# Kernel tuning notes

Measured on AMD Instinct MI355X. Metric: run time of the kernel, lower is better.

Reference implementation:

```python
import jax, jax.numpy as jnp
import numpy as np

B, S, D, H, F = 8, 1024, 1024, 16, 4096
DH = D // H  # 64
EPS = 1e-5


def layer_norm(x, g, b):
    mu = jnp.mean(x, axis=-1, keepdims=True)
    var = jnp.mean(jnp.square(x - mu), axis=-1, keepdims=True)
    return (x - mu) * jax.lax.rsqrt(var + EPS) * g + b


def mha(q_in, k_in, v_in, wq, wk, wv, wo, causal):
    # wq/wk/wv: [H, D, DH] (stacked per-head nn.Linear weights, pre-transposed)
    Q = jnp.einsum('bsd,hdk->bhsk', q_in, wq)
    K = jnp.einsum('bsd,hdk->bhsk', k_in, wk)
    V = jnp.einsum('bsd,hdk->bhsk', v_in, wv)
    scores = jnp.einsum('bhsk,bhtk->bhst', Q, K) / jnp.sqrt(jnp.asarray(DH, Q.dtype))
    if causal:
        mask = jnp.triu(jnp.ones((S, S), dtype=bool), k=1)  # True = inaccessible
        scores = jnp.where(mask, -jnp.inf, scores)
    A = jax.nn.softmax(scores, axis=-1)
    heads = jnp.einsum('bhst,bhtk->bhsk', A, V)
    heads = heads.transpose(0, 2, 1, 3).reshape(q_in.shape[0], q_in.shape[1], D)
    return heads @ wo.T  # nn.Linear convention


def setup_inputs() -> dict:
    key = jax.random.key(0)
    ks = jax.random.split(key, 16)
    sc = 1.0 / np.sqrt(D)
    scf = 1.0 / np.sqrt(F)
    return {
        'embeds': jax.random.normal(ks[0], (B, S, D), jnp.float32),
        'encoder_output': jax.random.normal(ks[1], (B, S, D), jnp.float32),
        'wq1': jax.random.normal(ks[2], (H, D, DH), jnp.float32) * sc,
        'wk1': jax.random.normal(ks[3], (H, D, DH), jnp.float32) * sc,
        'wv1': jax.random.normal(ks[4], (H, D, DH), jnp.float32) * sc,
        'wo1': jax.random.normal(ks[5], (D, D), jnp.float32) * sc,
        'wq2': jax.random.normal(ks[6], (H, D, DH), jnp.float32) * sc,
        'wk2': jax.random.normal(ks[7], (H, D, DH), jnp.float32) * sc,
        'wv2': jax.random.normal(ks[8], (H, D, DH), jnp.float32) * sc,
        'wo2': jax.random.normal(ks[9], (D, D), jnp.float32) * sc,
        'ln1_g': jnp.ones((D,), jnp.float32), 'ln1_b': jnp.zeros((D,), jnp.float32),
        'ln2_g': jnp.ones((D,), jnp.float32), 'ln2_b': jnp.zeros((D,), jnp.float32),
        'ln3_g': jnp.ones((D,), jnp.float32), 'ln3_b': jnp.zeros((D,), jnp.float32),
        'w1': jax.random.normal(ks[10], (F, D), jnp.float32) * sc,
        'b1': jnp.zeros((F,), jnp.float32),
        'w2': jax.random.normal(ks[11], (D, F), jnp.float32) * scf,
        'b2': jnp.zeros((D,), jnp.float32),
    }


def reference(embeds, encoder_output, wq1, wk1, wv1, wo1, wq2, wk2, wv2, wo2,
              ln1_g, ln1_b, ln2_g, ln2_b, ln3_g, ln3_b, w1, b1, w2, b2):
    # masked (causal) self-attention + residual + LN
    sa = mha(embeds, embeds, embeds, wq1, wk1, wv1, wo1, causal=True)
    x1 = layer_norm(sa + embeds, ln1_g, ln1_b)
    # cross-attention (no mask) + residual + LN
    ca = mha(x1, encoder_output, encoder_output, wq2, wk2, wv2, wo2, causal=False)
    x2 = layer_norm(ca + x1, ln2_g, ln2_b)
    # feedforward (Linear -> GELU(exact) -> Linear) + residual + LN
    ff = jax.nn.gelu(x2 @ w1.T + b1, approximate=False) @ w2.T + b2
    return layer_norm(ff + x2, ln3_g, ln3_b)
```

## Files before the change

kernel.cpp:

```cpp
#include <hip/hip_runtime.h>
#include <cstdint>
#include <cstddef>

typedef unsigned short u16;
typedef __attribute__((ext_vector_type(4))) float f32x4;
typedef __attribute__((ext_vector_type(4))) float f4;
typedef __attribute__((ext_vector_type(8))) short short8x;
typedef __attribute__((ext_vector_type(4))) u16 u16x4;
typedef __attribute__((ext_vector_type(8))) u16 u16x8;

#define DEV static __device__ __forceinline__

DEV void gl_lds16(const void* g, void* l) {
  __builtin_amdgcn_global_load_lds(
      (const __attribute__((address_space(1))) unsigned int*)g,
      (__attribute__((address_space(3))) unsigned int*)l, 16, 0, 0);
}

DEV u16 f2bf(float f) {
  unsigned u = __float_as_uint(f);
  u += 0x7fffu + ((u >> 16) & 1u);
  return (u16)(u >> 16);
}


__global__ __launch_bounds__(256) void cast_bf16(const float* __restrict__ X, u16* __restrict__ Y) {
  size_t i = ((size_t)blockIdx.x * 256 + threadIdx.x) * 4;
  f4 v = *(const f4*)(X + i);
  u16x4 y;
#pragma unroll
  for (int j = 0; j < 4; ++j) y[j] = f2bf(v[j]);
  *(u16x4*)(Y + i) = y;
}

__global__ __launch_bounds__(256) void cast_wqkv(const float* __restrict__ W, u16* __restrict__ Wt) {
  __shared__ float tile[64][65];
  const int t = threadIdx.x;
  const int h = blockIdx.y;
  const int d0 = blockIdx.x * 64;
  const float* Wb = W + (size_t)h * (1024 * 64);
  const int di = t >> 2;
  const int j0 = (t & 3) * 16;
#pragma unroll
  for (int c = 0; c < 4; ++c) {
    f4 v = *(const f4*)(Wb + (size_t)(d0 + di) * 64 + j0 + c * 4);
#pragma unroll
    for (int j = 0; j < 4; ++j) tile[di][j0 + c * 4 + j] = v[j];
  }
  __syncthreads();
  const int k = t >> 2;
  const int dd0 = (t & 3) * 16;
  u16x8 o0, o1;
#pragma unroll
  for (int u = 0; u < 8; ++u) o0[u] = f2bf(tile[dd0 + u][k]);
#pragma unroll
  for (int u = 0; u < 8; ++u) o1[u] = f2bf(tile[dd0 + 8 + u][k]);
  u16* dst = Wt + (size_t)(h * 64 + k) * 1024 + d0 + dd0;
  *(u16x8*)(dst) = o0;
  *(u16x8*)(dst + 8) = o1;
}

__global__ __launch_bounds__(256) void transpose_v(const u16* __restrict__ V, u16* __restrict__ Vt,
                                                   int vstride, int voff) {
  __shared__ u16 tile[32][72];
  const int t = threadIdx.x;
  const int bh = blockIdx.y;
  const int s0 = blockIdx.x * 32;
  const u16* Vb = V + (size_t)(bh >> 4) * (1024 * (size_t)vstride) + voff + (bh & 15) * 64;
  const int si = t >> 3, d0 = (t & 7) * 8;
  u16x8 val = *(const u16x8*)(Vb + (size_t)(s0 + si) * vstride + d0);
#pragma unroll
  for (int u = 0; u < 8; ++u) tile[si][d0 + u] = val[u];
  __syncthreads();
  const int d = t >> 2, sj0 = (t & 3) * 8;
  u16x8 o;
#pragma unroll
  for (int u = 0; u < 8; ++u) o[u] = tile[sj0 + u][d];
  *(u16x8*)(Vt + (size_t)bh * (64 * 1024) + (size_t)d * 1024 + s0 + sj0) = o;
}

template <int EPI>
__global__ __launch_bounds__(256, 3) void gemm_bt(const u16* __restrict__ A, const u16* __restrict__ Bt,
                                                  void* __restrict__ C, const float* __restrict__ bias,
                                                  int Krow, int Kit, int ldc, long long zC) {
  __shared__ u16 As0[128 * 32], Bs0[128 * 32];
  __shared__ u16 As1[128 * 32], Bs1[128 * 32];
  const int t = threadIdx.x;
  const int wave = t >> 6, lane = t & 63;
  const int lr = lane & 15, lkg = lane >> 4;
  const int swz = (lr >> 1) & 3;
  const int wr = (wave >> 1) * 64, wc = (wave & 1) * 64;

  const int gx = gridDim.x;
  const int nwg = gx * gridDim.y;
  const int flat = blockIdx.y * gx + blockIdx.x;
  const int wg = (flat & 7) * (nwg >> 3) + (flat >> 3);
  const int m0 = (wg / gx) * 128, n0 = (wg % gx) * 128;

  const int schunk = ((t & 3) ^ ((t >> 3) & 3)) << 4;
  const size_t rowb = (size_t)Krow * 2;
  const size_t rowskip = (size_t)64 * rowb;
  const size_t zoff = (size_t)blockIdx.z * (size_t)Kit * 2;
  const char* gA0 = (const char*)A + (size_t)(m0 + (t >> 2)) * rowb + zoff + schunk;
  const char* gA1 = gA0 + rowskip;
  const char* gB0 = (const char*)Bt + (size_t)(n0 + (t >> 2)) * rowb + zoff + schunk;
  const char* gB1 = gB0 + rowskip;

  char* dA0 = (char*)As0 + wave * 1024;
  char* dB0 = (char*)Bs0 + wave * 1024;
  char* dA1 = (char*)As1 + wave * 1024;
  char* dB1 = (char*)Bs1 + wave * 1024;

  const int aoff = (wr + lr) * 64 + ((lkg ^ swz) << 4);
  const int boff = (wc + lr) * 64 + ((lkg ^ swz) << 4);
  const char* rA0 = (const char*)As0 + aoff;
  const char* rB0 = (const char*)Bs0 + boff;
  const char* rA1 = (const char*)As1 + aoff;
  const char* rB1 = (const char*)Bs1 + boff;

  const f32x4 fzero = {0.f, 0.f, 0.f, 0.f};
  f32x4 acc[4][4];
#pragma unroll
  for (int m = 0; m < 4; ++m)
#pragma unroll
    for (int n = 0; n < 4; ++n) acc[m][n] = fzero;

  auto compute = [&](const char* rA, const char* rB) {
    short8x aF[4], bF[4];
#pragma unroll
    for (int m = 0; m < 4; ++m) aF[m] = *(const short8x*)(rA + m * 1024);
#pragma unroll
    for (int n = 0; n < 4; ++n) bF[n] = *(const short8x*)(rB + n * 1024);
#pragma unroll
    for (int m = 0; m < 4; ++m)
#pragma unroll
      for (int n = 0; n < 4; ++n)
        acc[m][n] = __builtin_amdgcn_mfma_f32_16x16x32_bf16(aF[m], bF[n], acc[m][n], 0, 0, 0);
  };

  gl_lds16(gA0, dA0); gl_lds16(gA1, dA0 + 4096);
  gl_lds16(gB0, dB0); gl_lds16(gB1, dB0 + 4096);
  gA0 += 64; gA1 += 64; gB0 += 64; gB1 += 64;
  __syncthreads();

  const int nk2 = Kit >> 6;
  for (int p = 0; p < nk2; ++p) {
    gl_lds16(gA0, dA1); gl_lds16(gA1, dA1 + 4096);
    gl_lds16(gB0, dB1); gl_lds16(gB1, dB1 + 4096);
    gA0 += 64; gA1 += 64; gB0 += 64; gB1 += 64;
    compute(rA0, rB0);
    __syncthreads();
    if (p + 1 < nk2) {
      gl_lds16(gA0, dA0); gl_lds16(gA1, dA0 + 4096);
      gl_lds16(gB0, dB0); gl_lds16(gB1, dB0 + 4096);
    }
    gA0 += 64; gA1 += 64; gB0 += 64; gB1 += 64;
    compute(rA1, rB1);
    __syncthreads();
  }

#pragma unroll
  for (int m = 0; m < 4; ++m) {
#pragma unroll
    for (int rr = 0; rr < 4; ++rr) {
      const int gm = m0 + wr + m * 16 + lkg * 4 + rr;
#pragma unroll
      for (int n = 0; n < 4; ++n) {
        const int gn = n0 + wc + n * 16 + lr;
        float v = acc[m][n][rr];
        if (EPI == 2 || EPI == 3) v += bias[gn];
        if (EPI == 2) v = 0.5f * v * (1.0f + erff(v * 0.70710678118654752f));
        if (EPI == 4) v *= 0.125f;
        if (EPI == 5 && gn < 1024) v *= 0.125f;
        if (EPI == 1 || EPI == 3)
          ((float*)C)[(size_t)blockIdx.z * zC + (size_t)gm * ldc + gn] = v;
        else
          ((u16*)C)[(size_t)gm * ldc + gn] = f2bf(v);
      }
    }
  }
}

template <int CAUSAL>
__global__ __launch_bounds__(256, 2) void flash_attn(const u16* __restrict__ Q, const u16* __restrict__ Kk,
                                                     const u16* __restrict__ Vt, u16* __restrict__ O,
                                                     int qst) {
  __shared__ u16 Ks[2][64 * 64];
  __shared__ u16 Vs[2][64 * 64];
  __shared__ u16 Ps[4][32 * 72];
  const int t = threadIdx.x;
  const int wave = t >> 6, lane = t & 63;
  const int lr = lane & 15, lkg = lane >> 4, lk = lkg * 8;
  const int sw = lr & 7;
  const int bh = blockIdx.y;
  const size_t base = (size_t)(bh >> 4) * (1024 * (size_t)qst) + (bh & 15) * 64;
  const u16* Qb = Q + base;
  const u16* Kb = Kk + base;
  const u16* Vtb = Vt + (size_t)bh * (64 * 1024);
  u16* Ob = O + (size_t)(bh >> 4) * (1024 * 1024) + (bh & 15) * 64;
  const int qt = blockIdx.x * 128;
  const int qw = qt + wave * 32;

  const f32x4 fzero = {0.f, 0.f, 0.f, 0.f};
  short8x qf[2][2];
#pragma unroll
  for (int rb = 0; rb < 2; ++rb)
#pragma unroll
    for (int kk = 0; kk < 2; ++kk)
      qf[rb][kk] = *(const short8x*)(Qb + (size_t)(qw + rb * 16 + lr) * qst + kk * 32 + lk);

  float m_[2][4], l_[2][4];
  f32x4 o_[2][4];
#pragma unroll
  for (int rb = 0; rb < 2; ++rb) {
#pragma unroll
    for (int rr = 0; rr < 4; ++rr) { m_[rb][rr] = -1e30f; l_[rb][rr] = 0.f; }
#pragma unroll
    for (int db = 0; db < 4; ++db) o_[rb][db] = fzero;
  }

  const int rsel = lane >> 3;
  const int csw = ((lane & 7) ^ rsel) << 4;

  auto stage = [&](int buf, int kv0) {
#pragma unroll
    for (int s = 0; s < 2; ++s) {
      const int row = s * 32 + wave * 8 + rsel;
      gl_lds16((const char*)Kb + (size_t)(kv0 + row) * (size_t)(qst * 2) + csw,
               (char*)&Ks[buf][0] + s * 4096 + wave * 1024);
      gl_lds16((const char*)Vtb + (size_t)row * 2048 + (size_t)kv0 * 2 + csw,
               (char*)&Vs[buf][0] + s * 4096 + wave * 1024);
    }
  };

  const int kv_end = CAUSAL ? (qt + 128) : 1024;
  const int nt = kv_end >> 6;

  stage(0, 0);
  __syncthreads();
  int cur = 0;
  for (int tt = 0; tt < nt; ++tt) {
    const int kv0 = tt * 64;
    if (tt + 1 < nt) stage(cur ^ 1, kv0 + 64);

    const char* ksb = (const char*)&Ks[cur][0];
    const char* vsb = (const char*)&Vs[cur][0];

    short8x kf[4][2];
#pragma unroll
    for (int nb = 0; nb < 4; ++nb) {
      const int row = nb * 16 + lr;
#pragma unroll
      for (int kk = 0; kk < 2; ++kk)
        kf[nb][kk] = *(const short8x*)(ksb + row * 128 + (((kk * 4 + lkg) ^ sw) << 4));
    }

#pragma unroll
    for (int rb = 0; rb < 2; ++rb) {
      f32x4 s[4];
#pragma unroll
      for (int nb = 0; nb < 4; ++nb) {
        s[nb] = __builtin_amdgcn_mfma_f32_16x16x32_bf16(qf[rb][0], kf[nb][0], fzero, 0, 0, 0);
        s[nb] = __builtin_amdgcn_mfma_f32_16x16x32_bf16(qf[rb][1], kf[nb][1], s[nb], 0, 0, 0);
      }
      if (CAUSAL && (kv0 + 63 > qw + rb * 16)) {
#pragma unroll
        for (int rr = 0; rr < 4; ++rr) {
          const int qg = qw + rb * 16 + lkg * 4 + rr;
#pragma unroll
          for (int nb = 0; nb < 4; ++nb)
            if (kv0 + nb * 16 + lr > qg) s[nb][rr] = -1e30f;
        }
      }
#pragma unroll
      for (int rr = 0; rr < 4; ++rr) {
        float mx = fmaxf(fmaxf(s[0][rr], s[1][rr]), fmaxf(s[2][rr], s[3][rr]));
#pragma unroll
        for (int d = 1; d < 16; d <<= 1) mx = fmaxf(mx, __shfl_xor(mx, d, 16));
        const float mold = m_[rb][rr];
        const float mnew = fmaxf(mold, mx);
        float p[4];
#pragma unroll
        for (int nb = 0; nb < 4; ++nb) p[nb] = __expf(s[nb][rr] - mnew);
        float rsum = (p[0] + p[1]) + (p[2] + p[3]);
#pragma unroll
        for (int d = 1; d < 16; d <<= 1) rsum += __shfl_xor(rsum, d, 16);
        const float alpha = __expf(mold - mnew);
        m_[rb][rr] = mnew;
        l_[rb][rr] = l_[rb][rr] * alpha + rsum;
#pragma unroll
        for (int db = 0; db < 4; ++db) o_[rb][db][rr] *= alpha;
        const int prow = rb * 16 + lkg * 4 + rr;
#pragma unroll
        for (int nb = 0; nb < 4; ++nb)
          Ps[wave][prow * 72 + nb * 16 + lr] = f2bf(p[nb]);
      }
    }
    asm volatile("s_waitcnt lgkmcnt(0)" ::: "memory");

    short8x vF[4][2];
#pragma unroll
    for (int db = 0; db < 4; ++db) {
      const int row = db * 16 + lr;
#pragma unroll
      for (int kk = 0; kk < 2; ++kk)
        vF[db][kk] = *(const short8x*)(vsb + row * 128 + (((kk * 4 + lkg) ^ sw) << 4));
    }
#pragma unroll
    for (int rb = 0; rb < 2; ++rb) {
#pragma unroll
      for (int kk = 0; kk < 2; ++kk) {
        const short8x aP = *(const short8x*)((const char*)&Ps[wave][0] + (rb * 16 + lr) * 144 + kk * 64 + lkg * 16);
#pragma unroll
        for (int db = 0; db < 4; ++db)
          o_[rb][db] = __builtin_amdgcn_mfma_f32_16x16x32_bf16(aP, vF[db][kk], o_[rb][db], 0, 0, 0);
      }
    }
    __syncthreads();
    cur ^= 1;
  }

#pragma unroll
  for (int rb = 0; rb < 2; ++rb)
#pragma unroll
    for (int rr = 0; rr < 4; ++rr) {
      const float inv = 1.0f / l_[rb][rr];
      const int qg = qw + rb * 16 + lkg * 4 + rr;
#pragma unroll
      for (int db = 0; db < 4; ++db)
        Ob[(size_t)qg * 1024 + db * 16 + lr] = f2bf(o_[rb][db][rr] * inv);
    }
}

__global__ __launch_bounds__(256) void ln_res(const float* __restrict__ X, const float* __restrict__ X2,
                                              const float* __restrict__ bias, const float* __restrict__ R,
                                              const float* __restrict__ gam, const float* __restrict__ bet,
                                              float* __restrict__ oF, u16* __restrict__ oB) {
  __shared__ float red[8];
  const int row = blockIdx.x, t = threadIdx.x;
  const int wave = t >> 6, lane = t & 63;
  const size_t off = (size_t)row * 1024 + t * 4;
  f4 x = *(const f4*)(X + off);
  f4 r = *(const f4*)(R + off);
  float v[4];
#pragma unroll
  for (int j = 0; j < 4; ++j) v[j] = x[j] + r[j];
  if (X2) {
    f4 x2 = *(const f4*)(X2 + off);
#pragma unroll
    for (int j = 0; j < 4; ++j) v[j] += x2[j];
  }
  if (bias) {
    f4 bb = *(const f4*)(bias + t * 4);
#pragma unroll
    for (int j = 0; j < 4; ++j) v[j] += bb[j];
  }
  float s = 0.f, sq = 0.f;
#pragma unroll
  for (int j = 0; j < 4; ++j) { s += v[j]; sq += v[j] * v[j]; }
#pragma unroll
  for (int d = 1; d < 64; d <<= 1) {
    s += __shfl_xor(s, d, 64);
    sq += __shfl_xor(sq, d, 64);
  }
  if (lane == 0) { red[wave * 2] = s; red[wave * 2 + 1] = sq; }
  __syncthreads();
  s = red[0] + red[2] + red[4] + red[6];
  sq = red[1] + red[3] + red[5] + red[7];
  const float mu = s * (1.0f / 1024.0f);
  const float var = sq * (1.0f / 1024.0f) - mu * mu;
  const float rs = rsqrtf(var + 1e-5f);
  f4 g4 = *(const f4*)(gam + t * 4);
  f4 b4 = *(const f4*)(bet + t * 4);
  f4 y;
#pragma unroll
  for (int j = 0; j < 4; ++j) y[j] = (v[j] - mu) * rs * g4[j] + b4[j];
  *(f4*)(oF + off) = y;
  if (oB) {
    u16x4 yb;
#pragma unroll
    for (int j = 0; j < 4; ++j) yb[j] = f2bf(y[j]);
    *(u16x4*)(oB + off) = yb;
  }
}

extern "C" void kernel_launch(void* const* d_in, const int* in_sizes, int n_in,
                              void* d_out, int out_size, void* d_ws, size_t ws_size,
                              hipStream_t stream) {
  const float* embeds = (const float*)d_in[0];
  const float* enc = (const float*)d_in[1];
  const float* wq1 = (const float*)d_in[2];
  const float* wk1 = (const float*)d_in[3];
  const float* wv1 = (const float*)d_in[4];
  const float* wo1 = (const float*)d_in[5];
  const float* wq2 = (const float*)d_in[6];
  const float* wk2 = (const float*)d_in[7];
  const float* wv2 = (const float*)d_in[8];
  const float* wo2 = (const float*)d_in[9];
  const float* ln1g = (const float*)d_in[10];
  const float* ln1b = (const float*)d_in[11];
  const float* ln2g = (const float*)d_in[12];
  const float* ln2b = (const float*)d_in[13];
  const float* ln3g = (const float*)d_in[14];
  const float* ln3b = (const float*)d_in[15];
  const float* w1 = (const float*)d_in[16];
  const float* b1 = (const float*)d_in[17];
  const float* w2 = (const float*)d_in[18];
  const float* b2 = (const float*)d_in[19];
  float* out = (float*)d_out;
  char* ws = (char*)d_ws;
  const size_t MB = (size_t)1 << 20;

  u16* QKV = (u16*)(ws + 0 * MB);
  u16* Vtb = (u16*)(ws + 48 * MB);
  u16* Hd = (u16*)(ws + 64 * MB);
  float* Of = (float*)(ws + 80 * MB);
  u16* ebf = (u16*)(ws + 112 * MB);
  u16* encb = (u16*)(ws + 128 * MB);
  float* x1f = (float*)(ws + 144 * MB);
  float* x2f = (float*)(ws + 176 * MB);
  u16* Wq1t = (u16*)(ws + 208 * MB);
  u16* Wk1t = (u16*)(ws + 210 * MB);
  u16* Wv1t = (u16*)(ws + 212 * MB);
  u16* Wo1b = (u16*)(ws + 214 * MB);
  u16* Wq2t = (u16*)(ws + 216 * MB);
  u16* Wk2t = (u16*)(ws + 218 * MB);
  u16* Wv2t = (u16*)(ws + 220 * MB);
  u16* Wo2b = (u16*)(ws + 222 * MB);
  u16* W1b = (u16*)(ws + 224 * MB);
  u16* W2b = (u16*)(ws + 232 * MB);
  u16* x1b = ebf;
  u16* x2b = encb;
  u16* Hff = (u16*)(ws + 0 * MB);

  float* P0 = (float*)(ws + 0 * MB);
  float* P3 = (float*)(ws + 112 * MB);
  const long long ZC = (long long)8192 * 1024;

  dim3 blk(256);

  cast_bf16<<<8192, blk, 0, stream>>>(embeds, ebf);
  cast_bf16<<<8192, blk, 0, stream>>>(enc, encb);
  cast_wqkv<<<dim3(16, 16), blk, 0, stream>>>(wq1, Wq1t);
  cast_wqkv<<<dim3(16, 16), blk, 0, stream>>>(wk1, Wk1t);
  cast_wqkv<<<dim3(16, 16), blk, 0, stream>>>(wv1, Wv1t);
  cast_wqkv<<<dim3(16, 16), blk, 0, stream>>>(wq2, Wq2t);
  cast_wqkv<<<dim3(16, 16), blk, 0, stream>>>(wk2, Wk2t);
  cast_wqkv<<<dim3(16, 16), blk, 0, stream>>>(wv2, Wv2t);
  cast_bf16<<<1024, blk, 0, stream>>>(wo1, Wo1b);
  cast_bf16<<<1024, blk, 0, stream>>>(wo2, Wo2b);
  cast_bf16<<<4096, blk, 0, stream>>>(w1, W1b);
  cast_bf16<<<4096, blk, 0, stream>>>(w2, W2b);

  gemm_bt<5><<<dim3(24, 64), blk, 0, stream>>>(ebf, Wq1t, QKV, nullptr, 1024, 1024, 3072, 0);
  transpose_v<<<dim3(32, 128), blk, 0, stream>>>(QKV, Vtb, 3072, 2048);
  flash_attn<1><<<dim3(8, 128), blk, 0, stream>>>(QKV, QKV + 1024, Vtb, Hd, 3072);
  gemm_bt<1><<<dim3(8, 64, 2), blk, 0, stream>>>(Hd, Wo1b, P0, nullptr, 1024, 512, 1024, ZC);
  ln_res<<<8192, blk, 0, stream>>>(P0, P0 + ZC, nullptr, embeds, ln1g, ln1b, x1f, x1b);

  gemm_bt<4><<<dim3(8, 64), blk, 0, stream>>>(x1b, Wq2t, QKV, nullptr, 1024, 1024, 3072, 0);
  gemm_bt<0><<<dim3(16, 64), blk, 0, stream>>>(encb, Wk2t, QKV + 1024, nullptr, 1024, 1024, 3072, 0);
  transpose_v<<<dim3(32, 128), blk, 0, stream>>>(QKV, Vtb, 3072, 2048);
  flash_attn<0><<<dim3(8, 128), blk, 0, stream>>>(QKV, QKV + 1024, Vtb, Hd, 3072);
  gemm_bt<1><<<dim3(8, 64, 2), blk, 0, stream>>>(Hd, Wo2b, P0, nullptr, 1024, 512, 1024, ZC);
  ln_res<<<8192, blk, 0, stream>>>(P0, P0 + ZC, nullptr, x1f, ln2g, ln2b, x2f, x2b);

  gemm_bt<2><<<dim3(32, 64), blk, 0, stream>>>(x2b, W1b, Hff, b1, 1024, 1024, 4096, 0);
  gemm_bt<1><<<dim3(8, 64, 2), blk, 0, stream>>>(Hff, W2b, Of, nullptr, 4096, 2048, 1024, ZC);
  ln_res<<<8192, blk, 0, stream>>>(Of, P3, b2, x2f, ln3g, ln3b, out, nullptr);
}
```

Measured before the change: 725.5 us.

## Deepen GEMM pipeline to four LDS stages with vmcnt waits and drop split-K for Wo

The GEMM main loop moves from a double-buffered scheme with __syncthreads to a four-stage LDS ring. Loads are issued two stages ahead and partial s_waitcnt vmcnt plus raw s_barrier are used, so more global loads stay in flight during MFMA work. LDS use doubles and the occupancy hint drops from 3 to 2 blocks per CU. The two attention output projections no longer use split-K over two z slices; they write a single fp32 result into Of, which cuts partial-sum traffic in LayerNorm but halves the grid for those GEMMs.

```diff
diff --git a/kernel.cpp b/kernel.cpp
--- a/kernel.cpp
+++ b/kernel.cpp
@@ -10,6 +10,10 @@
 typedef __attribute__((ext_vector_type(8))) u16 u16x8;
 
 #define DEV static __device__ __forceinline__
+#define VMC8() asm volatile("s_waitcnt vmcnt(8)" ::: "memory")
+#define VMC4() asm volatile("s_waitcnt vmcnt(4)" ::: "memory")
+#define VMC0() asm volatile("s_waitcnt vmcnt(0)" ::: "memory")
+#define BARR() asm volatile("s_barrier" ::: "memory")
 
 DEV void gl_lds16(const void* g, void* l) {
   __builtin_amdgcn_global_load_lds(
@@ -80,11 +84,11 @@
 }
 
 template <int EPI>
-__global__ __launch_bounds__(256, 3) void gemm_bt(const u16* __restrict__ A, const u16* __restrict__ Bt,
+__global__ __launch_bounds__(256, 2) void gemm_bt(const u16* __restrict__ A, const u16* __restrict__ Bt,
                                                   void* __restrict__ C, const float* __restrict__ bias,
                                                   int Krow, int Kit, int ldc, long long zC) {
-  __shared__ u16 As0[128 * 32], Bs0[128 * 32];
-  __shared__ u16 As1[128 * 32], Bs1[128 * 32];
+  __shared__ u16 As[4][128 * 32];
+  __shared__ u16 Bs[4][128 * 32];
   const int t = threadIdx.x;
   const int wave = t >> 6, lane = t & 63;
   const int lr = lane & 15, lkg = lane >> 4;
@@ -106,17 +110,8 @@
   const char* gB0 = (const char*)Bt + (size_t)(n0 + (t >> 2)) * rowb + zoff + schunk;
   const char* gB1 = gB0 + rowskip;
 
-  char* dA0 = (char*)As0 + wave * 1024;
-  char* dB0 = (char*)Bs0 + wave * 1024;
-  char* dA1 = (char*)As1 + wave * 1024;
-  char* dB1 = (char*)Bs1 + wave * 1024;
-
   const int aoff = (wr + lr) * 64 + ((lkg ^ swz) << 4);
   const int boff = (wc + lr) * 64 + ((lkg ^ swz) << 4);
-  const char* rA0 = (const char*)As0 + aoff;
-  const char* rB0 = (const char*)Bs0 + boff;
-  const char* rA1 = (const char*)As1 + aoff;
-  const char* rB1 = (const char*)Bs1 + boff;
 
   const f32x4 fzero = {0.f, 0.f, 0.f, 0.f};
   f32x4 acc[4][4];
@@ -125,7 +120,16 @@
 #pragma unroll
     for (int n = 0; n < 4; ++n) acc[m][n] = fzero;
 
-  auto compute = [&](const char* rA, const char* rB) {
+  auto stageBuf = [&](int b) {
+    char* da = (char*)&As[b][0] + wave * 1024;
+    char* db = (char*)&Bs[b][0] + wave * 1024;
+    gl_lds16(gA0, da); gl_lds16(gA1, da + 4096);
+    gl_lds16(gB0, db); gl_lds16(gB1, db + 4096);
+    gA0 += 64; gA1 += 64; gB0 += 64; gB1 += 64;
+  };
+  auto computeBuf = [&](int b) {
+    const char* rA = (const char*)&As[b][0] + aoff;
+    const char* rB = (const char*)&Bs[b][0] + boff;
     short8x aF[4], bF[4];
 #pragma unroll
     for (int m = 0; m < 4; ++m) aF[m] = *(const short8x*)(rA + m * 1024);
@@ -138,26 +142,21 @@
         acc[m][n] = __builtin_amdgcn_mfma_f32_16x16x32_bf16(aF[m], bF[n], acc[m][n], 0, 0, 0);
   };
 
-  gl_lds16(gA0, dA0); gl_lds16(gA1, dA0 + 4096);
-  gl_lds16(gB0, dB0); gl_lds16(gB1, dB0 + 4096);
-  gA0 += 64; gA1 += 64; gB0 += 64; gB1 += 64;
-  __syncthreads();
-
-  const int nk2 = Kit >> 6;
-  for (int p = 0; p < nk2; ++p) {
-    gl_lds16(gA0, dA1); gl_lds16(gA1, dA1 + 4096);
-    gl_lds16(gB0, dB1); gl_lds16(gB1, dB1 + 4096);
-    gA0 += 64; gA1 += 64; gB0 += 64; gB1 += 64;
-    compute(rA0, rB0);
-    __syncthreads();
-    if (p + 1 < nk2) {
-      gl_lds16(gA0, dA0); gl_lds16(gA1, dA0 + 4096);
-      gl_lds16(gB0, dB0); gl_lds16(gB1, dB0 + 4096);
-    }
-    gA0 += 64; gA1 += 64; gB0 += 64; gB1 += 64;
-    compute(rA1, rB1);
-    __syncthreads();
-  }
+  stageBuf(0); stageBuf(1);
+
+  const int nq = Kit >> 7;
+  for (int q = 0; q < nq - 1; ++q) {
+#pragma unroll
+    for (int j = 0; j < 4; ++j) {
+      stageBuf((j + 2) & 3);
+      VMC8(); BARR();
+      computeBuf(j);
+    }
+  }
+  stageBuf(2); VMC8(); BARR(); computeBuf(0);
+  stageBuf(3); VMC8(); BARR(); computeBuf(1);
+  VMC4(); BARR(); computeBuf(2);
+  VMC0(); BARR(); computeBuf(3);
 
 #pragma unroll
   for (int m = 0; m < 4; ++m) {
@@ -168,11 +167,11 @@
       for (int n = 0; n < 4; ++n) {
         const int gn = n0 + wc + n * 16 + lr;
         float v = acc[m][n][rr];
-        if (EPI == 2 || EPI == 3) v += bias[gn];
+        if (EPI == 2) v += bias[gn];
         if (EPI == 2) v = 0.5f * v * (1.0f + erff(v * 0.70710678118654752f));
         if (EPI == 4) v *= 0.125f;
         if (EPI == 5 && gn < 1024) v *= 0.125f;
-        if (EPI == 1 || EPI == 3)
+        if (EPI == 1)
           ((float*)C)[(size_t)blockIdx.z * zC + (size_t)gm * ldc + gn] = v;
         else
           ((u16*)C)[(size_t)gm * ldc + gn] = f2bf(v);
@@ -433,7 +432,6 @@
   u16* x2b = encb;
   u16* Hff = (u16*)(ws + 0 * MB);
 
-  float* P0 = (float*)(ws + 0 * MB);
   float* P3 = (float*)(ws + 112 * MB);
   const long long ZC = (long long)8192 * 1024;
 
@@ -455,15 +453,15 @@
   gemm_bt<5><<<dim3(24, 64), blk, 0, stream>>>(ebf, Wq1t, QKV, nullptr, 1024, 1024, 3072, 0);
   transpose_v<<<dim3(32, 128), blk, 0, stream>>>(QKV, Vtb, 3072, 2048);
   flash_attn<1><<<dim3(8, 128), blk, 0, stream>>>(QKV, QKV + 1024, Vtb, Hd, 3072);
-  gemm_bt<1><<<dim3(8, 64, 2), blk, 0, stream>>>(Hd, Wo1b, P0, nullptr, 1024, 512, 1024, ZC);
-  ln_res<<<8192, blk, 0, stream>>>(P0, P0 + ZC, nullptr, embeds, ln1g, ln1b, x1f, x1b);
+  gemm_bt<1><<<dim3(8, 64), blk, 0, stream>>>(Hd, Wo1b, Of, nullptr, 1024, 1024, 1024, 0);
+  ln_res<<<8192, blk, 0, stream>>>(Of, nullptr, nullptr, embeds, ln1g, ln1b, x1f, x1b);
 
   gemm_bt<4><<<dim3(8, 64), blk, 0, stream>>>(x1b, Wq2t, QKV, nullptr, 1024, 1024, 3072, 0);
   gemm_bt<0><<<dim3(16, 64), blk, 0, stream>>>(encb, Wk2t, QKV + 1024, nullptr, 1024, 1024, 3072, 0);
   transpose_v<<<dim3(32, 128), blk, 0, stream>>>(QKV, Vtb, 3072, 2048);
   flash_attn<0><<<dim3(8, 128), blk, 0, stream>>>(QKV, QKV + 1024, Vtb, Hd, 3072);
-  gemm_bt<1><<<dim3(8, 64, 2), blk, 0, stream>>>(Hd, Wo2b, P0, nullptr, 1024, 512, 1024, ZC);
-  ln_res<<<8192, blk, 0, stream>>>(P0, P0 + ZC, nullptr, x1f, ln2g, ln2b, x2f, x2b);
+  gemm_bt<1><<<dim3(8, 64), blk, 0, stream>>>(Hd, Wo2b, Of, nullptr, 1024, 1024, 1024, 0);
+  ln_res<<<8192, blk, 0, stream>>>(Of, nullptr, nullptr, x1f, ln2g, ln2b, x2f, x2b);
 
   gemm_bt<2><<<dim3(32, 64), blk, 0, stream>>>(x2b, W1b, Hff, b1, 1024, 1024, 4096, 0);
   gemm_bt<1><<<dim3(8, 64, 2), blk, 0, stream>>>(Hff, W2b, Of, nullptr, 4096, 2048, 1024, ZC);
```

Result: slower. 771.5 us (+6.3%).
